# Kernel optimization log

Hardware: AMD Instinct MI355X
Metric: run time of the kernel (lower is better)

## Reference

```python
import jax, jax.numpy as jnp
import numpy as np

TOP_K = 2
CAPACITY_FACTOR = 1.25
EPSILON = 1e-06
AUX_LOSS_WEIGHT = 0.01
NUM_EXPERTS = 64


def setup_inputs() -> dict:
    key = jax.random.key(0)
    k1, k2 = jax.random.split(key, 2)
    x = jax.random.normal(k1, (32768, 1024), dtype=jnp.float32)
    w_gate = jax.random.normal(k2, (NUM_EXPERTS, 1024), dtype=jnp.float32) * 0.02
    b_gate = jnp.zeros((NUM_EXPERTS,), dtype=jnp.float32)
    return {"x": x, "w_gate": w_gate, "b_gate": b_gate}


def reference(x, w_gate, b_gate):
    # x: [N, dim]; w_gate: [E, dim]; b_gate: [E]
    n_tokens = x.shape[0]
    capacity = int(CAPACITY_FACTOR * n_tokens)  # static, like torch int(...)

    logits = jnp.einsum('nd,ed->ne', x, w_gate) + b_gate          # [N, E]
    raw_gate_scores = jax.nn.softmax(logits, axis=-1)             # [N, E]

    _, top_k_indices = jax.lax.top_k(raw_gate_scores, TOP_K)      # [N, k]
    rows = jnp.arange(n_tokens)[:, None]                          # [N, 1]
    mask = jnp.zeros_like(raw_gate_scores).at[rows, top_k_indices].set(1.0)

    masked_gate_scores = raw_gate_scores * mask                   # [N, E]
    denominators = masked_gate_scores.sum(axis=0, keepdims=True) + EPSILON
    gate_scores = masked_gate_scores / denominators * capacity    # [N, E]

    importance = raw_gate_scores.mean(axis=0)                     # [E]
    load = mask.mean(axis=0)                                      # [E]
    aux_loss = AUX_LOSS_WEIGHT * (importance * load).mean() * (NUM_EXPERTS ** 2)
    return gate_scores, aux_loss
```

## Files before the change

kernel.cpp:

```cpp
#include <hip/hip_runtime.h>
#include <cstdint>

constexpr int N_TOK = 32768;
constexpr int DIM   = 1024;
constexpr int NEXP  = 64;
constexpr float CAPACITY = 40960.0f;
constexpr float EPS_DEN  = 1e-6f;

__device__ float  g_sums[256];
__device__ float4 g_rec[N_TOK];

__global__ void init_sums() {
    if (threadIdx.x < 192) g_sums[threadIdx.x] = 0.0f;
}

#define WAVES 4
#define RPW   8
#define ROWS_PER_BLK (WAVES * RPW)
#define BK    64

__global__ __launch_bounds__(256, 4)
void gate_main(const float* __restrict__ x,
               const float* __restrict__ wg,
               const float* __restrict__ bg) {
    __shared__ float4 wt[BK / 4][NEXP];
    __shared__ float4 xs[WAVES][RPW][BK / 4];

    const int tid  = threadIdx.x;
    const int lane = tid & 63;
    const int wv   = tid >> 6;
    const int row0 = blockIdx.x * ROWS_PER_BLK + wv * RPW;

    float acc[RPW];
#pragma unroll
    for (int r = 0; r < RPW; ++r) acc[r] = 0.0f;

    const float4* x4 = (const float4*)x;
    const float4* w4 = (const float4*)wg;

    for (int kt = 0; kt < DIM / BK; ++kt) {
        __syncthreads();
#pragma unroll
        for (int i = 0; i < 4; ++i) {
            int j  = tid + 256 * i;
            int k4 = j & 15;
            int e  = j >> 4;
            float4 val = w4[(size_t)e * (DIM / 4) + kt * (BK / 4) + k4];
            wt[k4][e ^ (k4 & 7)] = val;
        }
#pragma unroll
        for (int i = 0; i < 2; ++i) {
            int m  = lane + 64 * i;
            int r  = m >> 4;
            int c4 = m & 15;
            xs[wv][r][c4] = x4[(size_t)(row0 + r) * (DIM / 4) + kt * (BK / 4) + c4];
        }
        __syncthreads();

#pragma unroll
        for (int k4 = 0; k4 < BK / 4; ++k4) {
            float4 wvv = wt[k4][lane ^ (k4 & 7)];
#pragma unroll
            for (int r = 0; r < RPW; ++r) {
                float4 xv = xs[wv][r][k4];
                acc[r] = fmaf(xv.x, wvv.x, acc[r]);
                acc[r] = fmaf(xv.y, wvv.y, acc[r]);
                acc[r] = fmaf(xv.z, wvv.z, acc[r]);
                acc[r] = fmaf(xv.w, wvv.w, acc[r]);
            }
        }
    }

    const float b = bg[lane];
    float den_acc = 0.0f, imp_acc = 0.0f, load_acc = 0.0f;

    for (int r = 0; r < RPW; ++r) {
        float v = acc[r] + b;

        float m = v;
#pragma unroll
        for (int off = 32; off; off >>= 1) m = fmaxf(m, __shfl_xor(m, off));

        float ev = expf(v - m);
        float s = ev;
#pragma unroll
        for (int off = 32; off; off >>= 1) s += __shfl_xor(s, off);

        float raw = ev / s;

        unsigned long long mk1 = __ballot(v == m);
        int idx1 = __ffsll(mk1) - 1;

        float v2 = (lane == idx1) ? -INFINITY : v;
        float m2 = v2;
#pragma unroll
        for (int off = 32; off; off >>= 1) m2 = fmaxf(m2, __shfl_xor(m2, off));
        unsigned long long mk2 = __ballot(v2 == m2);
        int idx2 = __ffsll(mk2) - 1;

        bool sel = (lane == idx1) || (lane == idx2);
        imp_acc += raw;
        if (sel) { den_acc += raw; load_acc += 1.0f; }

        float raw1 = __shfl(raw, idx1);
        float raw2 = __shfl(raw, idx2);
        if (lane == 0) {
            g_rec[row0 + r] = make_float4(raw1, raw2,
                                          __int_as_float(idx1), __int_as_float(idx2));
        }
    }

    atomicAdd(&g_sums[lane],       den_acc);
    atomicAdd(&g_sums[64 + lane],  imp_acc);
    atomicAdd(&g_sums[128 + lane], load_acc);
}

__global__ void finalize(float* __restrict__ out) {
    int e = threadIdx.x;
    float den  = g_sums[e];
    float imp  = g_sums[64 + e];
    float load = g_sums[128 + e];
    g_sums[192 + e] = CAPACITY / (den + EPS_DEN);

    float prod = imp * load;
#pragma unroll
    for (int off = 32; off; off >>= 1) prod += __shfl_xor(prod, off);

    if (e == 0) {
        float S = prod / ((float)N_TOK * (float)N_TOK);
        out[(size_t)N_TOK * NEXP] = 0.64f * S;
    }
}

__global__ __launch_bounds__(256)
void scatter_out(float* __restrict__ out) {
    __shared__ float scale_s[NEXP];
    int tid = threadIdx.x;
    if (tid < NEXP) scale_s[tid] = g_sums[192 + tid];
    __syncthreads();

    int row = blockIdx.x * 16 + (tid >> 4);
    int g   = tid & 15;

    float4 rec = g_rec[row];
    int i1 = __float_as_int(rec.z);
    int i2 = __float_as_int(rec.w);
    float s1 = rec.x * scale_s[i1];
    float s2 = rec.y * scale_s[i2];

    int base = g * 4;
    float4 o;
    o.x = (i1 == base + 0) ? s1 : ((i2 == base + 0) ? s2 : 0.0f);
    o.y = (i1 == base + 1) ? s1 : ((i2 == base + 1) ? s2 : 0.0f);
    o.z = (i1 == base + 2) ? s1 : ((i2 == base + 2) ? s2 : 0.0f);
    o.w = (i1 == base + 3) ? s1 : ((i2 == base + 3) ? s2 : 0.0f);

    ((float4*)out)[(size_t)row * 16 + g] = o;
}

extern "C" void kernel_launch(void* const* d_in, const int* in_sizes, int n_in,
                              void* d_out, int out_size, void* d_ws, size_t ws_size,
                              hipStream_t stream) {
    const float* x  = (const float*)d_in[0];
    const float* wg = (const float*)d_in[1];
    const float* bg = (const float*)d_in[2];
    float* out = (float*)d_out;

    hipLaunchKernelGGL(init_sums, dim3(1), dim3(256), 0, stream);
    hipLaunchKernelGGL(gate_main, dim3(N_TOK / ROWS_PER_BLK), dim3(256), 0, stream,
                       x, wg, bg);
    hipLaunchKernelGGL(finalize, dim3(1), dim3(64), 0, stream, out);
    hipLaunchKernelGGL(scatter_out, dim3(N_TOK / 16), dim3(256), 0, stream, out);
}
```

Before: 425.4 us.

## Double-buffer gate weights, read x directly, packed FMA, fold finalize into scatter

The gate GEMM now double-buffers the weight tile in LDS, prefetching the next tile into registers while computing the current one. It drops the x staging through shared memory in favour of wave-uniform direct global loads (scalar-broadcast style) feeding packed 2-wide FMAs. The separate finalize kernel is removed: every scatter block recomputes the per-expert scales and block 0 writes the aux loss. This saves a launch and sync overhead, but risks higher register pressure and uncached-style global x reads on every k-step.

```diff
diff --git a/kernel.cpp b/kernel.cpp
--- a/kernel.cpp
+++ b/kernel.cpp
@@ -1,5 +1,8 @@
 #include <hip/hip_runtime.h>
 #include <cstdint>
+
+typedef float f32x2 __attribute__((ext_vector_type(2)));
+typedef float f32x4 __attribute__((ext_vector_type(4)));
 
 constexpr int N_TOK = 32768;
 constexpr int DIM   = 1024;
@@ -18,56 +21,70 @@
 #define RPW   8
 #define ROWS_PER_BLK (WAVES * RPW)
 #define BK    64
+#define NKT   (DIM / BK)
 
 __global__ __launch_bounds__(256, 4)
 void gate_main(const float* __restrict__ x,
                const float* __restrict__ wg,
                const float* __restrict__ bg) {
-    __shared__ float4 wt[BK / 4][NEXP];
-    __shared__ float4 xs[WAVES][RPW][BK / 4];
+    __shared__ f32x4 wt[2][BK / 4][NEXP];
 
     const int tid  = threadIdx.x;
     const int lane = tid & 63;
-    const int wv   = tid >> 6;
+    const int wv   = __builtin_amdgcn_readfirstlane(tid >> 6);
     const int row0 = blockIdx.x * ROWS_PER_BLK + wv * RPW;
 
-    float acc[RPW];
+    const f32x4* w4 = (const f32x4*)wg;
+    f32x4 st[4];
+
 #pragma unroll
-    for (int r = 0; r < RPW; ++r) acc[r] = 0.0f;
+    for (int i = 0; i < 4; ++i) {
+        int j = tid + 256 * i; int e = j >> 4; int k4 = j & 15;
+        st[i] = w4[(size_t)e * (DIM / 4) + k4];
+    }
+#pragma unroll
+    for (int i = 0; i < 4; ++i) {
+        int j = tid + 256 * i; int e = j >> 4; int k4 = j & 15;
+        wt[0][k4][e ^ (k4 & 7)] = st[i];
+    }
+    __syncthreads();
 
-    const float4* x4 = (const float4*)x;
-    const float4* w4 = (const float4*)wg;
+    f32x2 acc[RPW];
+#pragma unroll
+    for (int r = 0; r < RPW; ++r) acc[r] = (f32x2){0.0f, 0.0f};
 
-    for (int kt = 0; kt < DIM / BK; ++kt) {
-        __syncthreads();
+    const float* xbase = x + (size_t)row0 * DIM;
+
+    for (int kt = 0; kt < NKT; ++kt) {
+        const int cb = kt & 1;
+        if (kt + 1 < NKT) {
 #pragma unroll
-        for (int i = 0; i < 4; ++i) {
-            int j  = tid + 256 * i;
-            int k4 = j & 15;
-            int e  = j >> 4;
-            float4 val = w4[(size_t)e * (DIM / 4) + kt * (BK / 4) + k4];
-            wt[k4][e ^ (k4 & 7)] = val;
+            for (int i = 0; i < 4; ++i) {
+                int j = tid + 256 * i; int e = j >> 4; int k4 = j & 15;
+                st[i] = w4[(size_t)e * (DIM / 4) + (kt + 1) * (BK / 4) + k4];
+            }
         }
 #pragma unroll
-        for (int i = 0; i < 2; ++i) {
-            int m  = lane + 64 * i;
-            int r  = m >> 4;
-            int c4 = m & 15;
-            xs[wv][r][c4] = x4[(size_t)(row0 + r) * (DIM / 4) + kt * (BK / 4) + c4];
-        }
-        __syncthreads();
-
-#pragma unroll
         for (int k4 = 0; k4 < BK / 4; ++k4) {
-            float4 wvv = wt[k4][lane ^ (k4 & 7)];
+            f32x4 wv4 = wt[cb][k4][lane ^ (k4 & 7)];
+            f32x2 wlo = {wv4.x, wv4.y};
+            f32x2 whi = {wv4.z, wv4.w};
 #pragma unroll
             for (int r = 0; r < RPW; ++r) {
-                float4 xv = xs[wv][r][k4];
-                acc[r] = fmaf(xv.x, wvv.x, acc[r]);
-                acc[r] = fmaf(xv.y, wvv.y, acc[r]);
-                acc[r] = fmaf(xv.z, wvv.z, acc[r]);
-                acc[r] = fmaf(xv.w, wvv.w, acc[r]);
+                const f32x2* xp = (const f32x2*)(xbase + (size_t)r * DIM
+                                                 + kt * BK + k4 * 4);
+                acc[r] = __builtin_elementwise_fma(xp[0], wlo, acc[r]);
+                acc[r] = __builtin_elementwise_fma(xp[1], whi, acc[r]);
             }
+        }
+        if (kt + 1 < NKT) {
+            __syncthreads();
+#pragma unroll
+            for (int i = 0; i < 4; ++i) {
+                int j = tid + 256 * i; int e = j >> 4; int k4 = j & 15;
+                wt[cb ^ 1][k4][e ^ (k4 & 7)] = st[i];
+            }
+            __syncthreads();
         }
     }
 
@@ -75,7 +92,7 @@
     float den_acc = 0.0f, imp_acc = 0.0f, load_acc = 0.0f;
 
     for (int r = 0; r < RPW; ++r) {
-        float v = acc[r] + b;
+        float v = acc[r].x + acc[r].y + b;
 
         float m = v;
 #pragma unroll
@@ -115,28 +132,23 @@
     atomicAdd(&g_sums[128 + lane], load_acc);
 }
 
-__global__ void finalize(float* __restrict__ out) {
-    int e = threadIdx.x;
-    float den  = g_sums[e];
-    float imp  = g_sums[64 + e];
-    float load = g_sums[128 + e];
-    g_sums[192 + e] = CAPACITY / (den + EPS_DEN);
-
-    float prod = imp * load;
-#pragma unroll
-    for (int off = 32; off; off >>= 1) prod += __shfl_xor(prod, off);
-
-    if (e == 0) {
-        float S = prod / ((float)N_TOK * (float)N_TOK);
-        out[(size_t)N_TOK * NEXP] = 0.64f * S;
-    }
-}
-
 __global__ __launch_bounds__(256)
 void scatter_out(float* __restrict__ out) {
     __shared__ float scale_s[NEXP];
     int tid = threadIdx.x;
-    if (tid < NEXP) scale_s[tid] = g_sums[192 + tid];
+    if (tid < NEXP) {
+        float den = g_sums[tid];
+        scale_s[tid] = CAPACITY / (den + EPS_DEN);
+        if (blockIdx.x == 0) {
+            float prod = g_sums[64 + tid] * g_sums[128 + tid];
+#pragma unroll
+            for (int off = 32; off; off >>= 1) prod += __shfl_xor(prod, off);
+            if (tid == 0) {
+                out[(size_t)N_TOK * NEXP] =
+                    0.64f * prod / ((float)N_TOK * (float)N_TOK);
+            }
+        }
+    }
     __syncthreads();
 
     int row = blockIdx.x * 16 + (tid >> 4);
@@ -169,6 +181,5 @@
     hipLaunchKernelGGL(init_sums, dim3(1), dim3(256), 0, stream);
     hipLaunchKernelGGL(gate_main, dim3(N_TOK / ROWS_PER_BLK), dim3(256), 0, stream,
                        x, wg, bg);
-    hipLaunchKernelGGL(finalize, dim3(1), dim3(64), 0, stream, out);
     hipLaunchKernelGGL(scatter_out, dim3(N_TOK / 16), dim3(256), 0, stream, out);
 }
```

After: 539.3 us. 1.27x slower.
